# Optimization experiments

Hardware: AMD Instinct MI355X
Metric: run time of the kernel (lower is better)

Reference implementation:

```python
import jax, jax.numpy as jnp
import numpy as np

N = 50000   # nodes
E = 150000  # edges
G = 256     # graphs in batch
H0, H1, H2, H3 = 8, 128, 256, 512


def _lin(key, fi, fo):
    return jax.random.normal(key, (fi, fo), dtype=jnp.float32) * (1.0 / np.sqrt(fi))


def setup_inputs() -> dict:
    key = jax.random.key(0)
    ks = jax.random.split(key, 12)
    x = jax.random.normal(ks[0], (N, H0), dtype=jnp.float32)
    edge_index = jax.random.randint(ks[1], (2, E), 0, N)
    edge_weight = jax.random.uniform(ks[2], (E,), dtype=jnp.float32)
    batch = jnp.sort(jax.random.randint(ks[3], (N,), 0, G))
    return {
        'x': x, 'edge_index': edge_index, 'edge_weight': edge_weight, 'batch': batch,
        'W1': _lin(ks[4], H0, H1), 'b1': jnp.zeros((H1,), jnp.float32),
        'W2': _lin(ks[5], H1, H2), 'b2': jnp.zeros((H2,), jnp.float32),
        'W3': _lin(ks[6], H2, H3), 'b3': jnp.zeros((H3,), jnp.float32),
        'Wfc': _lin(ks[7], H3, 1), 'bfc': jnp.zeros((1,), jnp.float32),
    }


def _gcn_conv(h, W, b, src, dst, ew, n):
    # h: [N, Fin] -> [N, Fout]; symmetric GCN normalization (self-loops already in src/dst/ew)
    h = h @ W                                             # [N, Fout]
    deg = jax.ops.segment_sum(ew, dst, num_segments=n)    # [N]
    dinv = jnp.where(deg > 0, jax.lax.rsqrt(deg), 0.0)
    norm = dinv[src] * ew * dinv[dst]                     # [E+N]
    msgs = h[src] * norm[:, None]                         # gather + scale
    out = jax.ops.segment_sum(msgs, dst, num_segments=n)  # scatter-add
    return out + b


def reference(x, edge_index, edge_weight, batch, W1, b1, W2, b2, W3, b3, Wfc, bfc):
    n = x.shape[0]
    loop = jnp.arange(n)
    src = jnp.concatenate([edge_index[0], loop])
    dst = jnp.concatenate([edge_index[1], loop])
    ew = jnp.concatenate([edge_weight, jnp.ones((n,), edge_weight.dtype)])

    h1 = jax.nn.relu(_gcn_conv(x, W1, b1, src, dst, ew, n))
    h2 = jax.nn.relu(_gcn_conv(h1, W2, b2, src, dst, ew, n))
    h3 = jax.nn.relu(_gcn_conv(h2, W3, b3, src, dst, ew, n))

    # global mean pool over graphs
    sums = jax.ops.segment_sum(h3, batch, num_segments=G)              # [G, H3]
    cnt = jax.ops.segment_sum(jnp.ones((n,), h3.dtype), batch, num_segments=G)
    pooled = sums / jnp.maximum(cnt, 1.0)[:, None]

    return jax.nn.sigmoid(pooled @ Wfc + bfc)              # [G, 1]
```

## Files before the change

kernel.cpp:

```cpp
#include <hip/hip_runtime.h>
#include <math.h>

typedef __attribute__((ext_vector_type(8))) short short8;
typedef __attribute__((ext_vector_type(4))) float floatx4;


__device__ __forceinline__ unsigned short f2bf(float f) {
    unsigned int u = __float_as_uint(f);
    unsigned int r = (u + 0x7fffu + ((u >> 16) & 1u)) >> 16;
    return (unsigned short)r;
}
__device__ __forceinline__ float bfu_lo(unsigned int u) {
    return __uint_as_float(u << 16);
}
__device__ __forceinline__ float bfu_hi(unsigned int u) {
    return __uint_as_float(u & 0xffff0000u);
}


__global__ void k_init(float* __restrict__ deg, int* __restrict__ cnt,
                       int* __restrict__ cursor, int N) {
    int i = blockIdx.x * blockDim.x + threadIdx.x;
    if (i < N) { deg[i] = 1.0f; cnt[i] = 0; cursor[i] = 0; }
}

__global__ void k_hist_deg(const int* __restrict__ dst, const float* __restrict__ ew,
                           float* __restrict__ deg, int* __restrict__ cnt, int E) {
    int e = blockIdx.x * blockDim.x + threadIdx.x;
    if (e < E) {
        int d = dst[e];
        atomicAdd(&deg[d], ew[e]);
        atomicAdd(&cnt[d], 1);
    }
}

__global__ __launch_bounds__(256) void k_dinv_scana(float* __restrict__ deg,
                                                    const int* __restrict__ cnt,
                                                    int* __restrict__ bsum, int N) {
    int b = blockIdx.x, t = threadIdx.x;
    int base = b * 1024 + t * 4;
    int s = 0;
#pragma unroll
    for (int j = 0; j < 4; ++j) {
        int i = base + j;
        if (i < N) { deg[i] = rsqrtf(deg[i]); s += cnt[i]; }
    }
    __shared__ int sh[256];
    sh[t] = s; __syncthreads();
    for (int st = 128; st > 0; st >>= 1) { if (t < st) sh[t] += sh[t + st]; __syncthreads(); }
    if (t == 0) bsum[b] = sh[0];
}

__global__ __launch_bounds__(256) void k_scan_b(int* __restrict__ bsum, int nb) {
    int t = threadIdx.x;
    __shared__ int sh[256];
    int orig = (t < nb) ? bsum[t] : 0;
    sh[t] = orig; __syncthreads();
    for (int off = 1; off < 256; off <<= 1) {
        int x = (t >= off) ? sh[t - off] : 0;
        __syncthreads();
        sh[t] += x;
        __syncthreads();
    }
    if (t < nb) bsum[t] = sh[t] - orig;
}

__global__ __launch_bounds__(256) void k_scan_c(const int* __restrict__ cnt,
                                                const int* __restrict__ boff,
                                                int* __restrict__ row_start, int N) {
    int b = blockIdx.x, t = threadIdx.x;
    int base = b * 1024 + t * 4;
    int v[4]; int s = 0;
#pragma unroll
    for (int j = 0; j < 4; ++j) { int i = base + j; v[j] = (i < N) ? cnt[i] : 0; s += v[j]; }
    __shared__ int sh[256];
    sh[t] = s; __syncthreads();
    for (int off = 1; off < 256; off <<= 1) {
        int x = (t >= off) ? sh[t - off] : 0;
        __syncthreads();
        sh[t] += x;
        __syncthreads();
    }
    int excl = sh[t] - s + boff[b];
#pragma unroll
    for (int j = 0; j < 4; ++j) {
        int i = base + j;
        if (i < N) row_start[i] = excl;
        excl += v[j];
        if (i == N - 1) row_start[N] = excl;
    }
}

__global__ void k_scatter_norm(const int* __restrict__ src, const int* __restrict__ dst,
                               const float* __restrict__ ew, const float* __restrict__ dinv,
                               const int* __restrict__ row_start, int* __restrict__ cursor,
                               int* __restrict__ esrc, float* __restrict__ enorm, int E) {
    int e = blockIdx.x * blockDim.x + threadIdx.x;
    if (e >= E) return;
    int d = dst[e], s = src[e];
    int pos = row_start[d] + atomicAdd(&cursor[d], 1);
    esrc[pos] = s;
    enorm[pos] = dinv[s] * ew[e] * dinv[d];
}


__global__ void k_wt_all(const float* __restrict__ W2, unsigned short* __restrict__ WT2,
                         int K2, int F2,
                         const float* __restrict__ W3, unsigned short* __restrict__ WT3,
                         int K3, int F3) {
    int gid = blockIdx.x * blockDim.x + threadIdx.x;
    int n2 = K2 * F2;
    if (gid < n2) {
        int k = gid / F2, n = gid % F2;
        WT2[(size_t)n * K2 + k] = f2bf(W2[gid]);
    } else {
        gid -= n2;
        if (gid >= K3 * F3) return;
        int k = gid / F3, n = gid % F3;
        WT3[(size_t)n * K3 + k] = f2bf(W3[gid]);
    }
}


__global__ __launch_bounds__(256) void k_l1_gemm(
    const float* __restrict__ x, const float* __restrict__ dinv,
    const int* __restrict__ esrc, const float* __restrict__ enorm,
    const int* __restrict__ row_start, const float* __restrict__ W1,
    const float* __restrict__ b1, unsigned short* __restrict__ h1, int N) {
    __shared__ float As[8][132];
    __shared__ float Bs[8][128];

    int tid = threadIdx.x;
    int bm = blockIdx.x * 128;

#pragma unroll
    for (int i = tid; i < 1024; i += 256) Bs[i >> 7][i & 127] = W1[i];

    if (tid < 128) {
        int n = bm + tid;
        float a[8] = {0, 0, 0, 0, 0, 0, 0, 0};
        if (n < N) {
            float dv = dinv[n];
            float dv2 = dv * dv;
            float4 v0 = *(const float4*)&x[(size_t)n * 8];
            float4 v1 = *(const float4*)&x[(size_t)n * 8 + 4];
            a[0] = v0.x * dv2; a[1] = v0.y * dv2; a[2] = v0.z * dv2; a[3] = v0.w * dv2;
            a[4] = v1.x * dv2; a[5] = v1.y * dv2; a[6] = v1.z * dv2; a[7] = v1.w * dv2;
            int j1 = row_start[n + 1];
            for (int j = row_start[n]; j < j1; ++j) {
                int s = esrc[j];
                float w = enorm[j];
                float4 u0 = *(const float4*)&x[(size_t)s * 8];
                float4 u1 = *(const float4*)&x[(size_t)s * 8 + 4];
                a[0] += w * u0.x; a[1] += w * u0.y; a[2] += w * u0.z; a[3] += w * u0.w;
                a[4] += w * u1.x; a[5] += w * u1.y; a[6] += w * u1.z; a[7] += w * u1.w;
            }
        }
#pragma unroll
        for (int k = 0; k < 8; ++k) As[k][tid] = a[k];
    }
    __syncthreads();

    int tx = tid & 15;
    int ty = tid >> 4;
    float acc[8][8];
#pragma unroll
    for (int i = 0; i < 8; ++i)
#pragma unroll
        for (int j = 0; j < 8; ++j) acc[i][j] = 0.f;

#pragma unroll
    for (int k = 0; k < 8; ++k) {
        float a[8], b[8];
        float4 a0 = *(const float4*)&As[k][ty * 4];
        float4 a1 = *(const float4*)&As[k][ty * 4 + 64];
        float4 b0 = *(const float4*)&Bs[k][tx * 4];
        float4 b1 = *(const float4*)&Bs[k][tx * 4 + 64];
        a[0] = a0.x; a[1] = a0.y; a[2] = a0.z; a[3] = a0.w;
        a[4] = a1.x; a[5] = a1.y; a[6] = a1.z; a[7] = a1.w;
        b[0] = b0.x; b[1] = b0.y; b[2] = b0.z; b[3] = b0.w;
        b[4] = b1.x; b[5] = b1.y; b[6] = b1.z; b[7] = b1.w;
#pragma unroll
        for (int i = 0; i < 8; ++i)
#pragma unroll
            for (int j = 0; j < 8; ++j) acc[i][j] += a[i] * b[j];
    }

    float4 bi0 = *(const float4*)&b1[tx * 4];
    float4 bi1 = *(const float4*)&b1[tx * 4 + 64];
    float bb[8] = {bi0.x, bi0.y, bi0.z, bi0.w, bi1.x, bi1.y, bi1.z, bi1.w};
#pragma unroll
    for (int i = 0; i < 8; ++i) {
        int gm = bm + ((i < 4) ? (ty * 4 + i) : (64 + ty * 4 + i - 4));
        if (gm >= N) continue;
        ushort4 v0, v1;
        v0.x = f2bf(fmaxf(acc[i][0] + bb[0], 0.f));
        v0.y = f2bf(fmaxf(acc[i][1] + bb[1], 0.f));
        v0.z = f2bf(fmaxf(acc[i][2] + bb[2], 0.f));
        v0.w = f2bf(fmaxf(acc[i][3] + bb[3], 0.f));
        v1.x = f2bf(fmaxf(acc[i][4] + bb[4], 0.f));
        v1.y = f2bf(fmaxf(acc[i][5] + bb[5], 0.f));
        v1.z = f2bf(fmaxf(acc[i][6] + bb[6], 0.f));
        v1.w = f2bf(fmaxf(acc[i][7] + bb[7], 0.f));
        *(ushort4*)&h1[(size_t)gm * 128 + tx * 4] = v0;
        *(ushort4*)&h1[(size_t)gm * 128 + tx * 4 + 64] = v1;
    }
}


__global__ void k_agg_bf(const unsigned short* __restrict__ h, const float* __restrict__ dinv,
                         const int* __restrict__ esrc, const float* __restrict__ enorm,
                         const int* __restrict__ row_start,
                         unsigned short* __restrict__ A,
                         int N, int Mpad, int F, int osh) {
    int p = blockIdx.x * blockDim.x + threadIdx.x;
    int oct = F >> 3;
    if (p >= Mpad * oct) return;
    int n = p >> osh;
    int fo = (p & (oct - 1)) << 3;
    size_t oidx = (size_t)n * F + fo;
    if (n >= N) {
        *(uint4*)&A[oidx] = make_uint4(0, 0, 0, 0);
        return;
    }
    float dv = dinv[n];
    float dv2 = dv * dv;
    uint4 hv = *(const uint4*)&h[oidx];
    float s0 = bfu_lo(hv.x) * dv2, s1 = bfu_hi(hv.x) * dv2;
    float s2 = bfu_lo(hv.y) * dv2, s3 = bfu_hi(hv.y) * dv2;
    float s4 = bfu_lo(hv.z) * dv2, s5 = bfu_hi(hv.z) * dv2;
    float s6 = bfu_lo(hv.w) * dv2, s7 = bfu_hi(hv.w) * dv2;
    int j1 = row_start[n + 1];
    for (int j = row_start[n]; j < j1; ++j) {
        int s = esrc[j];
        float w = enorm[j];
        uint4 nv = *(const uint4*)&h[(size_t)s * F + fo];
        s0 += w * bfu_lo(nv.x); s1 += w * bfu_hi(nv.x);
        s2 += w * bfu_lo(nv.y); s3 += w * bfu_hi(nv.y);
        s4 += w * bfu_lo(nv.z); s5 += w * bfu_hi(nv.z);
        s6 += w * bfu_lo(nv.w); s7 += w * bfu_hi(nv.w);
    }
    uint4 o;
    o.x = (unsigned int)f2bf(s0) | ((unsigned int)f2bf(s1) << 16);
    o.y = (unsigned int)f2bf(s2) | ((unsigned int)f2bf(s3) << 16);
    o.z = (unsigned int)f2bf(s4) | ((unsigned int)f2bf(s5) << 16);
    o.w = (unsigned int)f2bf(s6) | ((unsigned int)f2bf(s7) << 16);
    *(uint4*)&A[oidx] = o;
}


template <int EPI>
__global__ __launch_bounds__(256, 4) void k_gemm_async(
    const unsigned short* __restrict__ A, const unsigned short* __restrict__ B,
    const float* __restrict__ bias, unsigned short* __restrict__ C,
    const float* __restrict__ Wfc, float* __restrict__ part,
    int M, int Mpad, int K, int Fout, int nbsh) {
    __shared__ __align__(16) unsigned short smem[8192];

    int tid = threadIdx.x, wave = tid >> 6, lane = tid & 63;
    int quad = lane >> 4, r = lane & 15;

    int P = blockIdx.x;
    int r8 = P & 7;
    int q = P >> 3;
    int bnIdx = q & ((1 << nbsh) - 1);
    int g = ((q >> nbsh) << 3) + r8;
    int bm = g * 128, bn = bnIdx * 128;
    int wm = (wave & 1) * 64, wn = (wave >> 1) * 64;

    const unsigned short* gsrc[2] = {A, B};
    const int rb[2] = {bm, bn};

    floatx4 acc[4][4] = {};

    for (int k0 = 0; k0 < K; k0 += 32) {
#pragma unroll
        for (int t = 0; t < 2; ++t) {
#pragma unroll
            for (int i = 0; i < 2; ++i) {
                int qc = wave * 2 + i;
                int idx = qc * 64 + lane;
                int row = idx >> 2, kofs = (idx & 3) << 3;
                const unsigned short* gptr = gsrc[t] + ((size_t)(rb[t] + row) * K + k0 + kofs);
                unsigned short* l = &smem[t * 4096 + qc * 512];
                __builtin_amdgcn_global_load_lds(
                    (const __attribute__((address_space(1))) void*)gptr,
                    (__attribute__((address_space(3))) void*)l, 16, 0, 0);
            }
        }
        __syncthreads();

        short8 ah[4];
#pragma unroll
        for (int mt = 0; mt < 4; ++mt) {
            int m = wm + mt * 16 + r;
            ah[mt] = *(const short8*)&smem[m * 32 + quad * 8];
        }
#pragma unroll
        for (int nt = 0; nt < 4; ++nt) {
            int n = wn + nt * 16 + r;
            short8 bh = *(const short8*)&smem[4096 + n * 32 + quad * 8];
#pragma unroll
            for (int mt = 0; mt < 4; ++mt)
                acc[mt][nt] = __builtin_amdgcn_mfma_f32_16x16x32_bf16(ah[mt], bh, acc[mt][nt], 0, 0, 0);
        }
        __syncthreads();
    }

    float bv[4];
#pragma unroll
    for (int nt = 0; nt < 4; ++nt) bv[nt] = bias[bn + wn + nt * 16 + r];

    if (EPI == 0) {
        float* eps = (float*)&smem[0] + wave * 1024;
#pragma unroll
        for (int mt = 0; mt < 4; ++mt) {
#pragma unroll
            for (int nt = 0; nt < 4; ++nt)
#pragma unroll
                for (int reg = 0; reg < 4; ++reg)
                    eps[(quad * 4 + reg) * 64 + nt * 16 + r] =
                        fmaxf(acc[mt][nt][reg] + bv[nt], 0.f);
#pragma unroll
            for (int i = 0; i < 4; ++i) {
                int fl = i * 64 + lane;
                int ri = fl >> 4, c4 = fl & 15;
                float4 v = *(const float4*)&eps[ri * 64 + c4 * 4];
                int gm = bm + wm + mt * 16 + ri;
                if (gm < M)
                    *(ushort4*)&C[(size_t)gm * Fout + bn + wn + c4 * 4] =
                        make_ushort4(f2bf(v.x), f2bf(v.y), f2bf(v.z), f2bf(v.w));
            }
        }
    } else {
        float* rowsum = (float*)&smem[0];
        if (tid < 128) rowsum[tid] = 0.f;
        __syncthreads();
        float wf[4];
#pragma unroll
        for (int nt = 0; nt < 4; ++nt) wf[nt] = Wfc[bn + wn + nt * 16 + r];
#pragma unroll
        for (int mt = 0; mt < 4; ++mt)
#pragma unroll
            for (int reg = 0; reg < 4; ++reg) {
                float v = 0.f;
#pragma unroll
                for (int nt = 0; nt < 4; ++nt)
                    v += fmaxf(acc[mt][nt][reg] + bv[nt], 0.f) * wf[nt];
                v += __shfl_xor(v, 1);
                v += __shfl_xor(v, 2);
                v += __shfl_xor(v, 4);
                v += __shfl_xor(v, 8);
                if (r == 0) atomicAdd(&rowsum[wm + mt * 16 + quad * 4 + reg], v);
            }
        __syncthreads();
        if (tid < 128) part[(size_t)bnIdx * Mpad + bm + tid] = rowsum[tid];
    }
}


__global__ __launch_bounds__(256) void k_pool2(const float* __restrict__ part,
                                               const int* __restrict__ batch,
                                               const float* __restrict__ bfc,
                                               float* __restrict__ out,
                                               int N, int Mpad, int nchunks, int G) {
    int g = (int)((blockIdx.x * blockDim.x + threadIdx.x) >> 6);
    int lane = threadIdx.x & 63;
    if (g >= G) return;
    int lo = 0, hi = N;
    while (lo < hi) { int m = (lo + hi) >> 1; if (batch[m] < g) lo = m + 1; else hi = m; }
    int start = lo;
    hi = N;
    while (lo < hi) { int m = (lo + hi) >> 1; if (batch[m] < g + 1) lo = m + 1; else hi = m; }
    int end = lo;
    float s = 0.f;
    for (int i = start + lane; i < end; i += 64) {
        float t = 0.f;
        for (int c = 0; c < nchunks; ++c) t += part[(size_t)c * Mpad + i];
        s += t;
    }
#pragma unroll
    for (int off = 32; off > 0; off >>= 1) s += __shfl_down(s, off);
    if (lane == 0) {
        float c = (float)(end - start);
        if (c < 1.f) c = 1.f;
        float z = s / c + bfc[0];
        out[g] = 1.f / (1.f + expf(-z));
    }
}


static inline int cdiv(int a, int b) { return (a + b - 1) / b; }

extern "C" void kernel_launch(void* const* d_in, const int* in_sizes, int n_in,
                              void* d_out, int out_size, void* d_ws, size_t ws_size,
                              hipStream_t stream) {
    const float* x   = (const float*)d_in[0];
    const int*   ei  = (const int*)d_in[1];
    const float* ew  = (const float*)d_in[2];
    const int*   bat = (const int*)d_in[3];
    const float* W1  = (const float*)d_in[4];
    const float* b1  = (const float*)d_in[5];
    const float* W2  = (const float*)d_in[6];
    const float* b2  = (const float*)d_in[7];
    const float* W3  = (const float*)d_in[8];
    const float* b3  = (const float*)d_in[9];
    const float* Wfc = (const float*)d_in[10];
    const float* bfc = (const float*)d_in[11];
    float* out = (float*)d_out;

    const int N  = in_sizes[3];
    const int E  = in_sizes[2];
    const int H1 = in_sizes[5];
    const int H2 = in_sizes[7];
    const int H3 = in_sizes[9];
    const int G  = out_size;
    const int Mpad = cdiv(N, 1024) * 1024;
    const int Npad4 = (N + 4) & ~3;

    const int* srcv = ei;
    const int* dstv = ei + E;

    char* p = (char*)d_ws;
    float* dinv      = (float*)p; p += (size_t)N * 4;
    int*   cnt       = (int*)p;   p += (size_t)N * 4;
    int*   cursor    = (int*)p;   p += (size_t)N * 4;
    int*   bsum      = (int*)p;   p += 256 * 4;
    int*   row_start = (int*)p;   p += (size_t)Npad4 * 4;
    int*   esrc      = (int*)p;   p += (size_t)E * 4;
    float* enorm     = (float*)p; p += (size_t)E * 4;
    float* part      = (float*)p; p += (size_t)(H3 / 128) * Mpad * 4;
    unsigned short* WT2 = (unsigned short*)p; p += (size_t)H1 * H2 * 2;
    unsigned short* WT3 = (unsigned short*)p; p += (size_t)H2 * H3 * 2;
    unsigned short* Abf = (unsigned short*)p; p += (size_t)Mpad * H2 * 2;
    unsigned short* h1  = (unsigned short*)p; p += (size_t)Mpad * H1 * 2;
    unsigned short* h2  = (unsigned short*)p; p += (size_t)Mpad * H2 * 2;

    k_init<<<cdiv(N, 256), 256, 0, stream>>>(dinv, cnt, cursor, N);
    k_hist_deg<<<cdiv(E, 256), 256, 0, stream>>>(dstv, ew, dinv, cnt, E);
    int nb = cdiv(N, 1024);
    k_dinv_scana<<<nb, 256, 0, stream>>>(dinv, cnt, bsum, N);
    k_scan_b<<<1, 256, 0, stream>>>(bsum, nb);
    k_scan_c<<<nb, 256, 0, stream>>>(cnt, bsum, row_start, N);
    k_scatter_norm<<<cdiv(E, 256), 256, 0, stream>>>(srcv, dstv, ew, dinv, row_start,
                                                     cursor, esrc, enorm, E);

    k_wt_all<<<cdiv(H1 * H2 + H2 * H3, 256), 256, 0, stream>>>(W2, WT2, H1, H2, W3, WT3, H2, H3);

    k_l1_gemm<<<cdiv(N, 128), 256, 0, stream>>>(x, dinv, esrc, enorm, row_start, W1, b1, h1, N);

    k_agg_bf<<<cdiv(Mpad * (H1 / 8), 256), 256, 0, stream>>>(
        h1, dinv, esrc, enorm, row_start, Abf, N, Mpad, H1, __builtin_ctz(H1) - 3);
    k_gemm_async<0><<<(Mpad / 128) * (H2 / 128), 256, 0, stream>>>(
        Abf, WT2, b2, h2, nullptr, nullptr, N, Mpad, H1, H2, __builtin_ctz(H2 / 128));

    k_agg_bf<<<cdiv(Mpad * (H2 / 8), 256), 256, 0, stream>>>(
        h2, dinv, esrc, enorm, row_start, Abf, N, Mpad, H2, __builtin_ctz(H2) - 3);
    k_gemm_async<1><<<(Mpad / 128) * (H3 / 128), 256, 0, stream>>>(
        Abf, WT3, b3, nullptr, Wfc, part, N, Mpad, H2, H3, __builtin_ctz(H3 / 128));

    k_pool2<<<cdiv(G * 64, 256), 256, 0, stream>>>(part, bat, bfc, out, N, Mpad, H3 / 128, G);
}
```

Before: 226.4 us.

## Merge graph preprocessing kernels into one cooperative kernel with grid syncs

Replaces the seven preprocessing launches (init, degree histogram, dinv plus block sums, block-sum scan, row-start scan, CSR scatter with norms, weight transpose) with a single cooperative kernel of 1024 blocks that separates phases with grid.sync(). The aim is to remove per-launch overhead and the idle gaps between several small kernels. In exchange it adds grid-wide barrier cost and a serial per-block tile scan over larger chunks. It also depends on all 1024 blocks being co-resident, which the cooperative launch requires.

```diff
diff --git a/kernel.cpp b/kernel.cpp
--- a/kernel.cpp
+++ b/kernel.cpp
@@ -1,8 +1,13 @@
 #include <hip/hip_runtime.h>
+#include <hip/hip_cooperative_groups.h>
 #include <math.h>
+
+namespace cg = cooperative_groups;
 
 typedef __attribute__((ext_vector_type(8))) short short8;
 typedef __attribute__((ext_vector_type(4))) float floatx4;
+
+#define GRID_PRE 1024
 
 
 __device__ __forceinline__ unsigned short f2bf(float f) {
@@ -18,106 +23,103 @@
 }
 
 
-__global__ void k_init(float* __restrict__ deg, int* __restrict__ cnt,
-                       int* __restrict__ cursor, int N) {
-    int i = blockIdx.x * blockDim.x + threadIdx.x;
-    if (i < N) { deg[i] = 1.0f; cnt[i] = 0; cursor[i] = 0; }
-}
-
-__global__ void k_hist_deg(const int* __restrict__ dst, const float* __restrict__ ew,
-                           float* __restrict__ deg, int* __restrict__ cnt, int E) {
-    int e = blockIdx.x * blockDim.x + threadIdx.x;
-    if (e < E) {
+__global__ __launch_bounds__(256, 4) void k_pre(
+    const int* __restrict__ src, const int* __restrict__ dst,
+    const float* __restrict__ ew,
+    const float* __restrict__ W2, const float* __restrict__ W3,
+    float* __restrict__ deg , int* __restrict__ cnt,
+    int* __restrict__ cursor, int* __restrict__ bsum,
+    int* __restrict__ row_start, int* __restrict__ esrc,
+    float* __restrict__ enorm,
+    unsigned short* __restrict__ WT2, unsigned short* __restrict__ WT3,
+    int N, int E, int K2, int F2, int K3, int F3) {
+    cg::grid_group grid = cg::this_grid();
+    const int t = threadIdx.x;
+    const int nb = gridDim.x;
+    const int gsz = nb * 256;
+    const int gt = blockIdx.x * 256 + t;
+    __shared__ int sh[256];
+
+    for (int i = gt; i < N; i += gsz) { deg[i] = 1.0f; cnt[i] = 0; cursor[i] = 0; }
+    int n2 = K2 * F2, n3 = K3 * F3;
+    for (int i = gt; i < n2; i += gsz) {
+        int k = i / F2, n = i % F2;
+        WT2[(size_t)n * K2 + k] = f2bf(W2[i]);
+    }
+    for (int i = gt; i < n3; i += gsz) {
+        int k = i / F3, n = i % F3;
+        WT3[(size_t)n * K3 + k] = f2bf(W3[i]);
+    }
+    grid.sync();
+
+    for (int e = gt; e < E; e += gsz) {
         int d = dst[e];
         atomicAdd(&deg[d], ew[e]);
         atomicAdd(&cnt[d], 1);
     }
-}
-
-__global__ __launch_bounds__(256) void k_dinv_scana(float* __restrict__ deg,
-                                                    const int* __restrict__ cnt,
-                                                    int* __restrict__ bsum, int N) {
-    int b = blockIdx.x, t = threadIdx.x;
-    int base = b * 1024 + t * 4;
+    grid.sync();
+
+    const int CH = (N + nb - 1) / nb;
+    const int b0 = blockIdx.x * CH;
+    const int b1 = min(N, b0 + CH);
     int s = 0;
-#pragma unroll
-    for (int j = 0; j < 4; ++j) {
-        int i = base + j;
-        if (i < N) { deg[i] = rsqrtf(deg[i]); s += cnt[i]; }
-    }
-    __shared__ int sh[256];
+    for (int i = b0 + t; i < b1; i += 256) { deg[i] = rsqrtf(deg[i]); s += cnt[i]; }
     sh[t] = s; __syncthreads();
     for (int st = 128; st > 0; st >>= 1) { if (t < st) sh[t] += sh[t + st]; __syncthreads(); }
-    if (t == 0) bsum[b] = sh[0];
-}
-
-__global__ __launch_bounds__(256) void k_scan_b(int* __restrict__ bsum, int nb) {
-    int t = threadIdx.x;
-    __shared__ int sh[256];
-    int orig = (t < nb) ? bsum[t] : 0;
-    sh[t] = orig; __syncthreads();
-    for (int off = 1; off < 256; off <<= 1) {
-        int x = (t >= off) ? sh[t - off] : 0;
+    if (t == 0) bsum[blockIdx.x] = sh[0];
+    grid.sync();
+
+    if (blockIdx.x == 0) {
+        int v[4]; int ls = 0;
+#pragma unroll
+        for (int j = 0; j < 4; ++j) {
+            int i = t * 4 + j;
+            v[j] = (i < nb) ? bsum[i] : 0;
+            ls += v[j];
+        }
+        sh[t] = ls; __syncthreads();
+        for (int off = 1; off < 256; off <<= 1) {
+            int x = (t >= off) ? sh[t - off] : 0;
+            __syncthreads();
+            sh[t] += x;
+            __syncthreads();
+        }
+        int excl = sh[t] - ls;
+#pragma unroll
+        for (int j = 0; j < 4; ++j) {
+            int i = t * 4 + j;
+            if (i < nb) bsum[i] = excl;
+            excl += v[j];
+        }
+    }
+    grid.sync();
+
+    int running = bsum[blockIdx.x];
+    for (int base = b0; base < b1; base += 256) {
+        int i = base + t;
+        int v = (i < b1) ? cnt[i] : 0;
+        sh[t] = v; __syncthreads();
+        for (int off = 1; off < 256; off <<= 1) {
+            int x = (t >= off) ? sh[t - off] : 0;
+            __syncthreads();
+            sh[t] += x;
+            __syncthreads();
+        }
+        if (i < b1) {
+            row_start[i] = running + sh[t] - v;
+            if (i == N - 1) row_start[N] = running + sh[t];
+        }
+        int tileTot = sh[255];
         __syncthreads();
-        sh[t] += x;
-        __syncthreads();
-    }
-    if (t < nb) bsum[t] = sh[t] - orig;
-}
-
-__global__ __launch_bounds__(256) void k_scan_c(const int* __restrict__ cnt,
-                                                const int* __restrict__ boff,
-                                                int* __restrict__ row_start, int N) {
-    int b = blockIdx.x, t = threadIdx.x;
-    int base = b * 1024 + t * 4;
-    int v[4]; int s = 0;
-#pragma unroll
-    for (int j = 0; j < 4; ++j) { int i = base + j; v[j] = (i < N) ? cnt[i] : 0; s += v[j]; }
-    __shared__ int sh[256];
-    sh[t] = s; __syncthreads();
-    for (int off = 1; off < 256; off <<= 1) {
-        int x = (t >= off) ? sh[t - off] : 0;
-        __syncthreads();
-        sh[t] += x;
-        __syncthreads();
-    }
-    int excl = sh[t] - s + boff[b];
-#pragma unroll
-    for (int j = 0; j < 4; ++j) {
-        int i = base + j;
-        if (i < N) row_start[i] = excl;
-        excl += v[j];
-        if (i == N - 1) row_start[N] = excl;
-    }
-}
-
-__global__ void k_scatter_norm(const int* __restrict__ src, const int* __restrict__ dst,
-                               const float* __restrict__ ew, const float* __restrict__ dinv,
-                               const int* __restrict__ row_start, int* __restrict__ cursor,
-                               int* __restrict__ esrc, float* __restrict__ enorm, int E) {
-    int e = blockIdx.x * blockDim.x + threadIdx.x;
-    if (e >= E) return;
-    int d = dst[e], s = src[e];
-    int pos = row_start[d] + atomicAdd(&cursor[d], 1);
-    esrc[pos] = s;
-    enorm[pos] = dinv[s] * ew[e] * dinv[d];
-}
-
-
-__global__ void k_wt_all(const float* __restrict__ W2, unsigned short* __restrict__ WT2,
-                         int K2, int F2,
-                         const float* __restrict__ W3, unsigned short* __restrict__ WT3,
-                         int K3, int F3) {
-    int gid = blockIdx.x * blockDim.x + threadIdx.x;
-    int n2 = K2 * F2;
-    if (gid < n2) {
-        int k = gid / F2, n = gid % F2;
-        WT2[(size_t)n * K2 + k] = f2bf(W2[gid]);
-    } else {
-        gid -= n2;
-        if (gid >= K3 * F3) return;
-        int k = gid / F3, n = gid % F3;
-        WT3[(size_t)n * K3 + k] = f2bf(W3[gid]);
+        running += tileTot;
+    }
+    grid.sync();
+
+    for (int e = gt; e < E; e += gsz) {
+        int d = dst[e], sidx = src[e];
+        int pos = row_start[d] + atomicAdd(&cursor[d], 1);
+        esrc[pos] = sidx;
+        enorm[pos] = deg[sidx] * ew[e] * deg[d];
     }
 }
 
@@ -409,12 +411,12 @@
     const float* bfc = (const float*)d_in[11];
     float* out = (float*)d_out;
 
-    const int N  = in_sizes[3];
-    const int E  = in_sizes[2];
-    const int H1 = in_sizes[5];
-    const int H2 = in_sizes[7];
-    const int H3 = in_sizes[9];
-    const int G  = out_size;
+    int N  = in_sizes[3];
+    int E  = in_sizes[2];
+    int H1 = in_sizes[5];
+    int H2 = in_sizes[7];
+    int H3 = in_sizes[9];
+    int G  = out_size;
     const int Mpad = cdiv(N, 1024) * 1024;
     const int Npad4 = (N + 4) & ~3;
 
@@ -425,7 +427,7 @@
     float* dinv      = (float*)p; p += (size_t)N * 4;
     int*   cnt       = (int*)p;   p += (size_t)N * 4;
     int*   cursor    = (int*)p;   p += (size_t)N * 4;
-    int*   bsum      = (int*)p;   p += 256 * 4;
+    int*   bsum      = (int*)p;   p += GRID_PRE * 4;
     int*   row_start = (int*)p;   p += (size_t)Npad4 * 4;
     int*   esrc      = (int*)p;   p += (size_t)E * 4;
     float* enorm     = (float*)p; p += (size_t)E * 4;
@@ -436,16 +438,16 @@
     unsigned short* h1  = (unsigned short*)p; p += (size_t)Mpad * H1 * 2;
     unsigned short* h2  = (unsigned short*)p; p += (size_t)Mpad * H2 * 2;
 
-    k_init<<<cdiv(N, 256), 256, 0, stream>>>(dinv, cnt, cursor, N);
-    k_hist_deg<<<cdiv(E, 256), 256, 0, stream>>>(dstv, ew, dinv, cnt, E);
-    int nb = cdiv(N, 1024);
-    k_dinv_scana<<<nb, 256, 0, stream>>>(dinv, cnt, bsum, N);
-    k_scan_b<<<1, 256, 0, stream>>>(bsum, nb);
-    k_scan_c<<<nb, 256, 0, stream>>>(cnt, bsum, row_start, N);
-    k_scatter_norm<<<cdiv(E, 256), 256, 0, stream>>>(srcv, dstv, ew, dinv, row_start,
-                                                     cursor, esrc, enorm, E);
-
-    k_wt_all<<<cdiv(H1 * H2 + H2 * H3, 256), 256, 0, stream>>>(W2, WT2, H1, H2, W3, WT3, H2, H3);
+    {
+        void* args[] = {
+            (void*)&srcv, (void*)&dstv, (void*)&ew, (void*)&W2, (void*)&W3,
+            (void*)&dinv, (void*)&cnt, (void*)&cursor, (void*)&bsum,
+            (void*)&row_start, (void*)&esrc, (void*)&enorm,
+            (void*)&WT2, (void*)&WT3,
+            (void*)&N, (void*)&E, (void*)&H1, (void*)&H2, (void*)&H2, (void*)&H3};
+        hipLaunchCooperativeKernel(reinterpret_cast<void*>(k_pre),
+                                   dim3(GRID_PRE), dim3(256), args, 0, stream);
+    }
 
     k_l1_gemm<<<cdiv(N, 128), 256, 0, stream>>>(x, dinv, esrc, enorm, row_start, W1, b1, h1, N);
 
```

Measured after the change: 744.1 us. +228.6%, slower.
